# Optimization experiments

Hardware: AMD Instinct MI355X
Metric: run time of the kernel (lower is better)

The kernel has to match this reference:

```python
import jax, jax.numpy as jnp
import numpy as np

IN_FEATURES = 2048
N_CONCEPTS = 64
EMB_SIZE = 128
BATCH = 8192
NEG_SLOPE = 0.01  # torch LeakyReLU default


def _leaky_relu(x):
    return jnp.where(x >= 0, x, NEG_SLOPE * x)


def setup_inputs() -> dict:
    key = jax.random.key(0)
    ks = jax.random.split(key, 7)
    s_e = 1.0 / np.sqrt(IN_FEATURES)
    s_c = 1.0 / np.sqrt(EMB_SIZE)
    s_p = 1.0 / np.sqrt(2 * EMB_SIZE)
    return {
        "x": jax.random.normal(ks[0], (BATCH, IN_FEATURES), jnp.float32),
        # embedder: Linear(in_features, emb_size)
        "We": jax.random.uniform(ks[1], (EMB_SIZE, IN_FEATURES), jnp.float32, -s_e, s_e),
        "be": jax.random.uniform(ks[2], (EMB_SIZE,), jnp.float32, -s_e, s_e),
        # per-concept generators: K x Linear(emb_size, 2*emb_size)
        "Wc": jax.random.uniform(ks[3], (N_CONCEPTS, 2 * EMB_SIZE, EMB_SIZE), jnp.float32, -s_c, s_c),
        "bc": jax.random.uniform(ks[4], (N_CONCEPTS, 2 * EMB_SIZE), jnp.float32, -s_c, s_c),
        # shared prob predictor: Linear(2*emb_size, 1)
        "wp": jax.random.uniform(ks[5], (2 * EMB_SIZE,), jnp.float32, -s_p, s_p),
        "bp": jax.random.uniform(ks[6], (1,), jnp.float32, -s_p, s_p),
    }


def reference(x, We, be, Wc, bc, wp, bp):
    # emb_pre: [B, E]
    emb = _leaky_relu(x @ We.T + be)
    # per-concept contexts, batched GEMM: [B, K, 2E]
    context = _leaky_relu(jnp.einsum("be,khe->bkh", emb, Wc) + bc)
    # concept probabilities: [B, K]
    c_pred = jax.nn.sigmoid(jnp.einsum("bkh,h->bk", context, wp) + bp[0])
    # no interventions (c=None) -> c_int == c_pred
    c_int = c_pred
    context_pos = context[:, :, :EMB_SIZE]
    context_neg = context[:, :, EMB_SIZE:]
    g = c_pred[:, :, None]
    c_emb = context_pos * g + context_neg * (1.0 - g)  # [B, K, E]
    return c_emb, c_pred, c_int, emb
```

## Files before the change

### kernel.cpp

```cpp
#include <hip/hip_runtime.h>
#include <hip/hip_bf16.h>

#define IN_F   2048
#define N_CON  64
#define EMB    128
#define BATCH  8192

#define CEMB_OFF  0
#define CPRED_OFF 67108864
#define CINT_OFF  67633152
#define EMB_OFF   68157440

typedef __attribute__((ext_vector_type(4))) float f32x4;
typedef __attribute__((ext_vector_type(8))) short short8;
typedef __attribute__((ext_vector_type(4))) short short4v;

#define MFMA16(A,B,C) __builtin_amdgcn_mfma_f32_16x16x32_bf16((A),(B),(C),0,0,0)

__device__ __forceinline__ short f2bf(float f) {
  unsigned u = __float_as_uint(f);
  u += 0x7FFFu + ((u >> 16) & 1u);
  return (short)(u >> 16);
}

__device__ __forceinline__ void gload_lds16(const void* g, void* l) {
  __builtin_amdgcn_global_load_lds(
      (const __attribute__((address_space(1))) unsigned*)g,
      (__attribute__((address_space(3))) unsigned*)l, 16, 0, 0);
}

__global__ void conv2_kernel(const float* __restrict__ a, short* __restrict__ da, int n4a,
                             const float* __restrict__ b, short* __restrict__ db, int n4b) {
  int i = blockIdx.x * blockDim.x + threadIdx.x;
  const float* s; short* d; int j;
  if (i < n4a)            { s = a; d = da; j = i; }
  else if (i < n4a + n4b) { s = b; d = db; j = i - n4a; }
  else return;
  f32x4 v = *(const f32x4*)(s + (size_t)j * 4);
  short4v o;
  o.x = f2bf(v.x); o.y = f2bf(v.y); o.z = f2bf(v.z); o.w = f2bf(v.w);
  *(short4v*)(d + (size_t)j * 4) = o;
}

__global__ __launch_bounds__(256, 4)
void gemm1_kernel(const float* __restrict__ x,
                  const short* __restrict__ we_bf,
                  const float* __restrict__ be,
                  float* __restrict__ out_emb,
                  short* __restrict__ emb_bf) {
  __shared__ short As[16 * 128];
  __shared__ short Bs[128 * 128];

  const int t = threadIdx.x;
  const int w = t >> 6, l = t & 63;
  const int row0 = blockIdx.x * 16;

  f32x4 acc[2];
  acc[0] = (f32x4){0.f, 0.f, 0.f, 0.f};
  acc[1] = (f32x4){0.f, 0.f, 0.f, 0.f};

  const int ar = t >> 4;
  const int aseg = t & 15;
  const float* xrow = x + (size_t)(row0 + ar) * IN_F + aseg * 8;
  short* adst = &As[ar * 128 + ((aseg * 8) ^ ((ar & 7) << 3))];

  const int brl = t >> 4;
  const int bseg = l & 15;

  for (int kt = 0; kt < 16; ++kt) {
    const int k0 = kt * 128;
    {
      f32x4 v0 = *(const f32x4*)(xrow + k0);
      f32x4 v1 = *(const f32x4*)(xrow + k0 + 4);
      short8 o;
      o[0] = f2bf(v0.x); o[1] = f2bf(v0.y); o[2] = f2bf(v0.z); o[3] = f2bf(v0.w);
      o[4] = f2bf(v1.x); o[5] = f2bf(v1.y); o[6] = f2bf(v1.z); o[7] = f2bf(v1.w);
      *(short8*)adst = o;
    }
#pragma unroll
    for (int i = 0; i < 8; ++i) {
      int n = i * 16 + brl;
      gload_lds16(we_bf + (size_t)n * IN_F + k0 + ((bseg ^ (n & 7)) * 8),
                  &Bs[i * 2048 + w * 512]);
    }
    __syncthreads();
#pragma unroll
    for (int ks = 0; ks < 4; ++ks) {
      int kcol = ks * 32 + ((l >> 4) << 3);
      int r0 = l & 15;
      short8 a = *(const short8*)&As[r0 * 128 + (kcol ^ ((r0 & 7) << 3))];
      int n0 = w * 32 + (l & 15), n1 = n0 + 16;
      short8 b0 = *(const short8*)&Bs[n0 * 128 + (kcol ^ ((n0 & 7) << 3))];
      short8 b1 = *(const short8*)&Bs[n1 * 128 + (kcol ^ ((n1 & 7) << 3))];
      acc[0] = MFMA16(a, b0, acc[0]);
      acc[1] = MFMA16(a, b1, acc[1]);
    }
    __syncthreads();
  }

#pragma unroll
  for (int nf = 0; nf < 2; ++nf) {
    int e = w * 32 + nf * 16 + (l & 15);
    float bev = be[e];
#pragma unroll
    for (int r = 0; r < 4; ++r) {
      int b = row0 + ((l >> 4) << 2) + r;
      float v = acc[nf][r] + bev;
      v = v >= 0.f ? v : 0.01f * v;
      out_emb[(size_t)b * EMB + e] = v;
      emb_bf[(size_t)b * EMB + e] = f2bf(v);
    }
  }
}

__global__ __launch_bounds__(256, 2)
void gemm2_kernel(const short* __restrict__ emb_bf,
                  const short* __restrict__ wc_bf,
                  const float* __restrict__ bc,
                  const float* __restrict__ wp,
                  const float* __restrict__ bp,
                  float* __restrict__ ws_pred,
                  float* __restrict__ out) {
  __shared__ short Bs[256 * 128];
  __shared__ short As[64 * 128];

  const int t = threadIdx.x;
  const int w = t >> 6, l = t & 63;
  const int kc = blockIdx.x & 63;
  const int mch = (blockIdx.x >> 6) * 512;

  float wph[16], bcv[16];
#pragma unroll
  for (int nf = 0; nf < 16; ++nf) {
    wph[nf] = wp[nf * 16 + (l & 15)];
    bcv[nf] = bc[kc * 256 + nf * 16 + (l & 15)];
  }
  const float bp0 = bp[0];

  const int rl = t >> 4;
  const int seg = l & 15;

#pragma unroll
  for (int i = 0; i < 16; ++i) {
    int rB = i * 16 + rl;
    gload_lds16(wc_bf + (size_t)kc * 32768 + (size_t)rB * 128 + ((seg ^ (rB & 7)) * 8),
                &Bs[i * 2048 + w * 512]);
  }
#pragma unroll
  for (int i = 0; i < 4; ++i) {
    int rA = i * 16 + rl;
    gload_lds16(emb_bf + (size_t)(mch + rA) * 128 + ((seg ^ (rA & 7)) * 8),
                &As[i * 2048 + w * 512]);
  }

  for (int it = 0; it < 8; ++it) {
    __syncthreads();

    f32x4 acc[16];
#pragma unroll
    for (int j = 0; j < 16; ++j) acc[j] = (f32x4){0.f, 0.f, 0.f, 0.f};

    const int r0 = w * 16 + (l & 15);
#pragma unroll
    for (int ks = 0; ks < 4; ++ks) {
      int kcol = ks * 32 + ((l >> 4) << 3);
      short8 a = *(const short8*)&As[r0 * 128 + (kcol ^ ((r0 & 7) << 3))];
#pragma unroll
      for (int nf = 0; nf < 16; ++nf) {
        int n = nf * 16 + (l & 15);
        short8 b = *(const short8*)&Bs[n * 128 + (kcol ^ ((n & 7) << 3))];
        acc[nf] = MFMA16(a, b, acc[nf]);
      }
    }
    __syncthreads();

    if (it < 7) {
#pragma unroll
      for (int i = 0; i < 4; ++i) {
        int rA = i * 16 + rl;
        gload_lds16(emb_bf + (size_t)(mch + (it + 1) * 64 + rA) * 128 + ((seg ^ (rA & 7)) * 8),
                    &As[i * 2048 + w * 512]);
      }
    }

    f32x4 p = (f32x4){0.f, 0.f, 0.f, 0.f};
#pragma unroll
    for (int nf = 0; nf < 16; ++nf) {
#pragma unroll
      for (int r = 0; r < 4; ++r) {
        float v = acc[nf][r] + bcv[nf];
        v = v >= 0.f ? v : 0.01f * v;
        acc[nf][r] = v;
        p[r] += v * wph[nf];
      }
    }
    float g[4];
#pragma unroll
    for (int r = 0; r < 4; ++r) {
      float s = p[r];
      s += __shfl_xor(s, 1);
      s += __shfl_xor(s, 2);
      s += __shfl_xor(s, 4);
      s += __shfl_xor(s, 8);
      g[r] = 1.f / (1.f + __expf(-(s + bp0)));
    }

    const int rowb = mch + it * 64 + w * 16 + ((l >> 4) << 2);
    if ((l & 15) == 0) {
      f32x4 gv; gv.x = g[0]; gv.y = g[1]; gv.z = g[2]; gv.w = g[3];
      *(f32x4*)&ws_pred[(size_t)kc * 8192 + rowb] = gv;
    }
#pragma unroll
    for (int r = 0; r < 4; ++r) {
      int brow = rowb + r;
      float gg = g[r];
#pragma unroll
      for (int nf = 0; nf < 8; ++nf) {
        float v = acc[nf][r] * gg + acc[nf + 8][r] * (1.f - gg);
        out[(size_t)brow * 8192 + kc * 128 + nf * 16 + (l & 15)] = v;
      }
    }
  }
}

__global__ __launch_bounds__(256)
void pred_tr_kernel(const float* __restrict__ ws_pred, float* __restrict__ out) {
  __shared__ float T[64][65];
  const int t = threadIdx.x;
  const int b0 = blockIdx.x * 64;

  {
    int kc = t >> 2;
    int j0 = (t & 3) * 16;
    const float* src = ws_pred + (size_t)kc * 8192 + b0 + j0;
#pragma unroll
    for (int i = 0; i < 4; ++i) {
      f32x4 v = *(const f32x4*)(src + i * 4);
      T[kc][j0 + i * 4 + 0] = v.x;
      T[kc][j0 + i * 4 + 1] = v.y;
      T[kc][j0 + i * 4 + 2] = v.z;
      T[kc][j0 + i * 4 + 3] = v.w;
    }
  }
  __syncthreads();
  {
    int bl = t & 63;
    int kq = (t >> 6) * 16;
#pragma unroll
    for (int i = 0; i < 4; ++i) {
      f32x4 v;
      v.x = T[kq + i * 4 + 0][bl];
      v.y = T[kq + i * 4 + 1][bl];
      v.z = T[kq + i * 4 + 2][bl];
      v.w = T[kq + i * 4 + 3][bl];
      *(f32x4*)&out[CPRED_OFF + (size_t)(b0 + bl) * 64 + kq + i * 4] = v;
      *(f32x4*)&out[CINT_OFF + (size_t)(b0 + bl) * 64 + kq + i * 4] = v;
    }
  }
}

extern "C" void kernel_launch(void* const* d_in, const int* in_sizes, int n_in,
                              void* d_out, int out_size, void* d_ws, size_t ws_size,
                              hipStream_t stream) {
  (void)in_sizes; (void)n_in; (void)out_size; (void)ws_size;
  const float* x  = (const float*)d_in[0];
  const float* We = (const float*)d_in[1];
  const float* be = (const float*)d_in[2];
  const float* Wc = (const float*)d_in[3];
  const float* bc = (const float*)d_in[4];
  const float* wp = (const float*)d_in[5];
  const float* bp = (const float*)d_in[6];
  float* out = (float*)d_out;

  short* we_bf  = (short*)d_ws;
  short* wc_bf  = we_bf + 262144;
  short* emb_bf = wc_bf + 2097152;
  float* ws_pred = (float*)(emb_bf + 1048576);

  conv2_kernel<<<2304, 256, 0, stream>>>(We, we_bf, 65536, Wc, wc_bf, 524288);
  gemm1_kernel<<<512, 256, 0, stream>>>(x, we_bf, be, out + EMB_OFF, emb_bf);
  gemm2_kernel<<<1024, 256, 0, stream>>>(emb_bf, wc_bf, bc, wp, bp, ws_pred, out);
  pred_tr_kernel<<<128, 256, 0, stream>>>(ws_pred, out);
}
```

Measured before the change: 124.5 us.

## Load emb A fragments directly to registers and double per-wave M tile in gemm2

The gemm2 kernel no longer stages emb rows through LDS. Each wave now loads its A fragments straight from global memory into registers and computes two 16-row M fragments per iteration, giving 4 iterations of 128 rows instead of 8 of 64. Each B fragment read from LDS is reused across two MFMAs, and the per-iteration __syncthreads barriers are removed. The bias is folded into the accumulator initialisation and the gate blend is rewritten as neg+(pos-neg)*g. In exchange the accumulators double to 128 floats per lane, which raises register pressure and may cut occupancy.

```diff
diff --git a/kernel.cpp b/kernel.cpp
--- a/kernel.cpp
+++ b/kernel.cpp
@@ -122,102 +122,100 @@
                   float* __restrict__ ws_pred,
                   float* __restrict__ out) {
   __shared__ short Bs[256 * 128];
-  __shared__ short As[64 * 128];
 
   const int t = threadIdx.x;
   const int w = t >> 6, l = t & 63;
   const int kc = blockIdx.x & 63;
   const int mch = (blockIdx.x >> 6) * 512;
 
-  float wph[16], bcv[16];
-#pragma unroll
-  for (int nf = 0; nf < 16; ++nf) {
-    wph[nf] = wp[nf * 16 + (l & 15)];
-    bcv[nf] = bc[kc * 256 + nf * 16 + (l & 15)];
-  }
-  const float bp0 = bp[0];
-
   const int rl = t >> 4;
   const int seg = l & 15;
-
 #pragma unroll
   for (int i = 0; i < 16; ++i) {
     int rB = i * 16 + rl;
     gload_lds16(wc_bf + (size_t)kc * 32768 + (size_t)rB * 128 + ((seg ^ (rB & 7)) * 8),
                 &Bs[i * 2048 + w * 512]);
   }
-#pragma unroll
-  for (int i = 0; i < 4; ++i) {
-    int rA = i * 16 + rl;
-    gload_lds16(emb_bf + (size_t)(mch + rA) * 128 + ((seg ^ (rA & 7)) * 8),
-                &As[i * 2048 + w * 512]);
-  }
-
-  for (int it = 0; it < 8; ++it) {
-    __syncthreads();
-
-    f32x4 acc[16];
-#pragma unroll
-    for (int j = 0; j < 16; ++j) acc[j] = (f32x4){0.f, 0.f, 0.f, 0.f};
-
-    const int r0 = w * 16 + (l & 15);
+
+  float wph[16], bcv[16];
+#pragma unroll
+  for (int nf = 0; nf < 16; ++nf) {
+    wph[nf] = wp[nf * 16 + (l & 15)];
+    bcv[nf] = bc[kc * 256 + nf * 16 + (l & 15)];
+  }
+  const float bp0 = bp[0];
+
+  __syncthreads();
+
+  const int lq = (l >> 4) << 3;
+
+  for (int it = 0; it < 4; ++it) {
+    const int rbase = mch + it * 128 + w * 32 + (l & 15);
+
+    short8 a[2][4];
+#pragma unroll
+    for (int mf = 0; mf < 2; ++mf)
+#pragma unroll
+      for (int ks = 0; ks < 4; ++ks)
+        a[mf][ks] = *(const short8*)&emb_bf[(size_t)(rbase + mf * 16) * 128 + ks * 32 + lq];
+
+    f32x4 acc[2][16];
+#pragma unroll
+    for (int mf = 0; mf < 2; ++mf)
+#pragma unroll
+      for (int nf = 0; nf < 16; ++nf)
+        acc[mf][nf] = (f32x4){bcv[nf], bcv[nf], bcv[nf], bcv[nf]};
+
 #pragma unroll
     for (int ks = 0; ks < 4; ++ks) {
-      int kcol = ks * 32 + ((l >> 4) << 3);
-      short8 a = *(const short8*)&As[r0 * 128 + (kcol ^ ((r0 & 7) << 3))];
+      int kcol = ks * 32 + lq;
 #pragma unroll
       for (int nf = 0; nf < 16; ++nf) {
         int n = nf * 16 + (l & 15);
         short8 b = *(const short8*)&Bs[n * 128 + (kcol ^ ((n & 7) << 3))];
-        acc[nf] = MFMA16(a, b, acc[nf]);
-      }
-    }
-    __syncthreads();
-
-    if (it < 7) {
-#pragma unroll
-      for (int i = 0; i < 4; ++i) {
-        int rA = i * 16 + rl;
-        gload_lds16(emb_bf + (size_t)(mch + (it + 1) * 64 + rA) * 128 + ((seg ^ (rA & 7)) * 8),
-                    &As[i * 2048 + w * 512]);
-      }
-    }
-
-    f32x4 p = (f32x4){0.f, 0.f, 0.f, 0.f};
-#pragma unroll
-    for (int nf = 0; nf < 16; ++nf) {
+        acc[0][nf] = MFMA16(a[0][ks], b, acc[0][nf]);
+        acc[1][nf] = MFMA16(a[1][ks], b, acc[1][nf]);
+      }
+    }
+
+#pragma unroll
+    for (int mf = 0; mf < 2; ++mf) {
+      f32x4 p = (f32x4){0.f, 0.f, 0.f, 0.f};
+#pragma unroll
+      for (int nf = 0; nf < 16; ++nf) {
+#pragma unroll
+        for (int r = 0; r < 4; ++r) {
+          float v = acc[mf][nf][r];
+          v = fmaxf(v, 0.01f * v);
+          acc[mf][nf][r] = v;
+          p[r] += v * wph[nf];
+        }
+      }
+      float g[4];
 #pragma unroll
       for (int r = 0; r < 4; ++r) {
-        float v = acc[nf][r] + bcv[nf];
-        v = v >= 0.f ? v : 0.01f * v;
-        acc[nf][r] = v;
-        p[r] += v * wph[nf];
-      }
-    }
-    float g[4];
-#pragma unroll
-    for (int r = 0; r < 4; ++r) {
-      float s = p[r];
-      s += __shfl_xor(s, 1);
-      s += __shfl_xor(s, 2);
-      s += __shfl_xor(s, 4);
-      s += __shfl_xor(s, 8);
-      g[r] = 1.f / (1.f + __expf(-(s + bp0)));
-    }
-
-    const int rowb = mch + it * 64 + w * 16 + ((l >> 4) << 2);
-    if ((l & 15) == 0) {
-      f32x4 gv; gv.x = g[0]; gv.y = g[1]; gv.z = g[2]; gv.w = g[3];
-      *(f32x4*)&ws_pred[(size_t)kc * 8192 + rowb] = gv;
-    }
-#pragma unroll
-    for (int r = 0; r < 4; ++r) {
-      int brow = rowb + r;
-      float gg = g[r];
-#pragma unroll
-      for (int nf = 0; nf < 8; ++nf) {
-        float v = acc[nf][r] * gg + acc[nf + 8][r] * (1.f - gg);
-        out[(size_t)brow * 8192 + kc * 128 + nf * 16 + (l & 15)] = v;
+        float s = p[r];
+        s += __shfl_xor(s, 1);
+        s += __shfl_xor(s, 2);
+        s += __shfl_xor(s, 4);
+        s += __shfl_xor(s, 8);
+        g[r] = 1.f / (1.f + __expf(-(s + bp0)));
+      }
+
+      const int rowb = mch + it * 128 + w * 32 + mf * 16 + ((l >> 4) << 2);
+      if ((l & 15) == 0) {
+        f32x4 gv; gv.x = g[0]; gv.y = g[1]; gv.z = g[2]; gv.w = g[3];
+        *(f32x4*)&ws_pred[(size_t)kc * 8192 + rowb] = gv;
+      }
+#pragma unroll
+      for (int r = 0; r < 4; ++r) {
+        int brow = rowb + r;
+        float gg = g[r];
+#pragma unroll
+        for (int nf = 0; nf < 8; ++nf) {
+          float pos = acc[mf][nf][r], neg = acc[mf][nf + 8][r];
+          out[(size_t)brow * 8192 + kc * 128 + nf * 16 + (l & 15)] = neg + (pos - neg) * gg;
+        }
       }
     }
   }
```

Result: slower. 417.4 us (+235.2%).
